# Kernel optimization log

Measured on AMD Instinct MI355X. Metric: run time of the kernel, lower is better.

## Reference

```python
import jax, jax.numpy as jnp
import numpy as np

BN_EPS = 1e-5


def conv1x1(x, w, b):
    # x: (B,C,H,W), w: (O,C), b: (O,)
    return jnp.einsum('bchw,oc->bohw', x, w) + b[None, :, None, None]


def maxpool2(x):
    # 2x2 max pool, stride 2; H,W assumed even
    B, C, H, W = x.shape
    return x.reshape(B, C, H // 2, 2, W // 2, 2).max(axis=(3, 5))


def setup_inputs() -> dict:
    key = jax.random.key(0)
    ks = jax.random.split(key, 8)
    B, C, Ci, H, W = 8, 256, 128, 64, 64
    s_in = 1.0 / np.sqrt(C)   # kaiming-uniform-ish scale for 1x1 convs
    s_ci = 1.0 / np.sqrt(Ci)
    return {
        'x': jax.random.normal(ks[0], (B, C, H, W), jnp.float32),
        'theta_w': jax.random.normal(ks[1], (Ci, C), jnp.float32) * s_in,
        'theta_b': jnp.zeros((Ci,), jnp.float32),
        'phi_w': jax.random.normal(ks[2], (Ci, C), jnp.float32) * s_in,
        'phi_b': jnp.zeros((Ci,), jnp.float32),
        'g_w': jax.random.normal(ks[3], (Ci, C), jnp.float32) * s_in,
        'g_b': jnp.zeros((Ci,), jnp.float32),
        'W_w': jax.random.normal(ks[4], (C, Ci), jnp.float32) * s_ci,
        'W_b': jnp.zeros((C,), jnp.float32),
        'bn_gamma': jnp.ones((C,), jnp.float32),
        'bn_beta': jnp.zeros((C,), jnp.float32),
    }


def reference(x, theta_w, theta_b, phi_w, phi_b, g_w, g_b, W_w, W_b, bn_gamma, bn_beta):
    B, C, H, W = x.shape
    Ci = theta_w.shape[0]
    # 1x1 conv projections
    theta = conv1x1(x, theta_w, theta_b).reshape(B, Ci, H * W)           # (B,Ci,N)
    phi = maxpool2(conv1x1(x, phi_w, phi_b)).reshape(B, Ci, -1)          # (B,Ci,M)
    g = maxpool2(conv1x1(x, g_w, g_b)).reshape(B, Ci, -1)                # (B,Ci,M)
    # attention: softmax(theta^T phi) g^T
    attn = jax.nn.softmax(jnp.einsum('bcn,bcm->bnm', theta, phi), axis=-1)  # (B,N,M)
    y = jnp.einsum('bnm,bcm->bcn', attn, g).reshape(B, Ci, H, W)
    # output projection + BatchNorm2d (training-mode batch stats) + residual
    y = conv1x1(y, W_w, W_b)
    mean = y.mean(axis=(0, 2, 3))
    var = y.var(axis=(0, 2, 3))
    y = (y - mean[None, :, None, None]) * jax.lax.rsqrt(var + BN_EPS)[None, :, None, None]
    y = y * bn_gamma[None, :, None, None] + bn_beta[None, :, None, None]
    return x + y
```

## Files before the change

### kernel.cpp

```cpp
#include <hip/hip_runtime.h>

#define B_ 8
#define C_ 256
#define CI_ 128
#define N_ 4096
#define M_ 1024

typedef unsigned short u16;
typedef unsigned int u32;
typedef _Float16 f16x8 __attribute__((ext_vector_type(8)));
typedef _Float16 f16x4 __attribute__((ext_vector_type(4)));
typedef float f32x4 __attribute__((ext_vector_type(4)));
typedef u16 u16x4 __attribute__((ext_vector_type(4)));
typedef u16 u16x8 __attribute__((ext_vector_type(8)));

__device__ __forceinline__ u16 f2h(float f) {
    _Float16 h = (_Float16)f;
    u16 u;
    __builtin_memcpy(&u, &h, 2);
    return u;
}
__device__ __forceinline__ float h2f(u16 u) {
    _Float16 h;
    __builtin_memcpy(&h, &u, 2);
    return (float)h;
}
__device__ __forceinline__ f16x8 ldh8(const u16* p) {
    return *reinterpret_cast<const f16x8*>(p);
}
__device__ __forceinline__ f32x4 MFMAH(f16x8 a, f16x8 b, f32x4 c) {
    return __builtin_amdgcn_mfma_f32_16x16x32_f16(a, b, c, 0, 0, 0);
}
__device__ __forceinline__ f32x4 MFMA16(f16x4 a, f16x4 b, f32x4 c) {
    return __builtin_amdgcn_mfma_f32_16x16x16f16(a, b, c, 0, 0, 0);
}
__device__ __forceinline__ void gld16(const u16* g, u16* l) {
    __builtin_amdgcn_global_load_lds(
        (const __attribute__((address_space(1))) void*)g,
        (__attribute__((address_space(3))) void*)l, 16, 0, 0);
}


__global__ __launch_bounds__(256) void k_prep(
    const float* __restrict__ tw, const float* __restrict__ tb,
    const float* __restrict__ pw, const float* __restrict__ pb,
    const float* __restrict__ gw, const float* __restrict__ gb,
    const float* __restrict__ Ww,
    u16* __restrict__ wcf, float* __restrict__ bcat, u16* __restrict__ wwf) {
    int idx = blockIdx.x * 256 + threadIdx.x;
    if (idx < 384 * 256) {
        int r = idx >> 8, c = idx & 255;
        float v = (r < 128) ? tw[r * 256 + c]
                : (r < 256) ? pw[(r - 128) * 256 + c]
                            : gw[(r - 256) * 256 + c];
        size_t off = (size_t)((r >> 4) * 8 + (c >> 5)) * 512 +
                     (((c >> 3) & 3) * 16 + (r & 15)) * 8 + (c & 7);
        wcf[off] = f2h(v);
    } else if (idx < 384 * 256 + 256 * 128) {
        int k2 = idx - 384 * 256;
        int c = k2 >> 7, k = k2 & 127;
        size_t off = (size_t)((c >> 4) * 4 + (k >> 5)) * 512 +
                     (((k >> 3) & 3) * 16 + (c & 15)) * 8 + (k & 7);
        wwf[off] = f2h(Ww[k2]);
    } else if (idx < 384 * 256 + 256 * 128 + 384) {
        int r = idx - (384 * 256 + 256 * 128);
        bcat[r] = (r < 128) ? tb[r] : (r < 256) ? pb[r - 128] : gb[r - 256];
    }
}

__global__ __launch_bounds__(256) void k_tx(const float* __restrict__ x,
                                            u16* __restrict__ xbf) {
    int bid = blockIdx.x;
    int b = bid >> 8, rem = bid & 255, nt = rem >> 2, ct = rem & 3;
    int n0 = nt * 64, c0 = ct * 64;
    __shared__ u16 th_[64][66];
    int j = threadIdx.x & 63, i0 = threadIdx.x >> 6;
    for (int i = i0; i < 64; i += 4)
        th_[i][j] = f2h(x[((size_t)b * C_ + c0 + i) * N_ + n0 + j]);
    __syncthreads();
    int w = threadIdx.x >> 6, lane = threadIdx.x & 63;
    int l15 = lane & 15, g16 = lane >> 4;
    int s = w;
#pragma unroll
    for (int kk = 0; kk < 2; ++kk) {
        u16x8 hv;
#pragma unroll
        for (int e = 0; e < 8; ++e)
            hv[e] = th_[kk * 32 + g16 * 8 + e][s * 16 + l15];
        size_t off = ((size_t)(b * 256 + (n0 >> 4) + s) * 8 + (c0 >> 5) + kk) * 512 +
                     (size_t)lane * 8;
        *(u16x8*)&xbf[off] = hv;
    }
}

__global__ __launch_bounds__(256) void k_proj(
    const u16* __restrict__ wcf, const float* __restrict__ bcat,
    const u16* __restrict__ xbf,
    u16* __restrict__ thf, u16* __restrict__ ppf, u16* __restrict__ gpf) {
    int bid = blockIdx.x;
    int b = bid / 96, rem = bid % 96, rt = rem >> 5, nt = rem & 31;
    int tid = threadIdx.x;
    int w = tid >> 6, lane = tid & 63;
    int l15 = lane & 15, g16 = lane >> 4;
    int wr = (w >> 1) * 64, wc = (w & 1) * 64;
    int rbase = rt * 128 + wr, nbase = nt * 128 + wc;
    __shared__ u16 tl[128][132];
    f32x4 acc[4][4];
#pragma unroll
    for (int i = 0; i < 4; ++i)
#pragma unroll
        for (int j = 0; j < 4; ++j)
#pragma unroll
            for (int r = 0; r < 4; ++r) acc[i][j][r] = 0.f;
#pragma unroll
    for (int ks = 0; ks < 8; ++ks) {
        f16x8 a[4], bb[4];
#pragma unroll
        for (int i = 0; i < 4; ++i)
            a[i] = ldh8(&wcf[((size_t)((rbase >> 4) + i) * 8 + ks) * 512 + (size_t)lane * 8]);
#pragma unroll
        for (int j = 0; j < 4; ++j)
            bb[j] = ldh8(&xbf[((size_t)(b * 256 + (nbase >> 4) + j) * 8 + ks) * 512 +
                              (size_t)lane * 8]);
#pragma unroll
        for (int i = 0; i < 4; ++i)
#pragma unroll
            for (int j = 0; j < 4; ++j) acc[i][j] = MFMAH(a[i], bb[j], acc[i][j]);
    }
    if (rt == 0) {
#pragma unroll
        for (int i = 0; i < 4; ++i) {
            int lrow = wr + i * 16 + g16 * 4;
#pragma unroll
            for (int j = 0; j < 4; ++j) {
                u16x4 pk;
#pragma unroll
                for (int r = 0; r < 4; ++r)
                    pk[r] = f2h(acc[i][j][r] + bcat[lrow + r]);
                size_t off = ((size_t)(b * 256 + (nbase >> 4) + j) * 4 + (lrow >> 5)) * 512 +
                             (((lrow >> 3) & 3) * 16 + l15) * 8 + (lrow & 7);
                *reinterpret_cast<u16x4*>(&thf[off]) = pk;
            }
        }
    } else {
#pragma unroll
        for (int i = 0; i < 4; ++i) {
            int lrow = wr + i * 16 + g16 * 4;
#pragma unroll
            for (int j = 0; j < 4; ++j) {
                int n_loc = wc + j * 16 + l15;
                u16x4 pk;
#pragma unroll
                for (int r = 0; r < 4; ++r)
                    pk[r] = f2h(acc[i][j][r] + bcat[rt * 128 + lrow + r]);
                *reinterpret_cast<u16x4*>(&tl[n_loc][lrow]) = pk;
            }
        }
        __syncthreads();
        if (rt == 1) {
#pragma unroll
            for (int half = 0; half < 2; ++half) {
                int w2 = (tid >> 4) + half * 16;
                int c8 = tid & 15;
                u16x8 v0 = *(const u16x8*)&tl[2 * w2][c8 * 8];
                u16x8 v1 = *(const u16x8*)&tl[2 * w2 + 1][c8 * 8];
                u16x8 v2 = *(const u16x8*)&tl[64 + 2 * w2][c8 * 8];
                u16x8 v3 = *(const u16x8*)&tl[65 + 2 * w2][c8 * 8];
                u16x8 o;
#pragma unroll
                for (int e = 0; e < 8; ++e) {
                    float mx = fmaxf(fmaxf(h2f(v0[e]), h2f(v1[e])),
                                     fmaxf(h2f(v2[e]), h2f(v3[e])));
                    o[e] = f2h(mx);
                }
                size_t off = ((size_t)(((b * 32 + nt) * 2 + (w2 >> 4)) * 4 + (c8 >> 2)) * 64 +
                              (c8 & 3) * 16 + (w2 & 15)) * 8;
                *(u16x8*)&ppf[off] = o;
            }
        } else {
#pragma unroll
            for (int s = 0; s < 2; ++s) {
                int wg = (tid >> 7) + s * 2;
                int ci = tid & 127;
                u16x4 o0, o1;
#pragma unroll
                for (int e = 0; e < 4; ++e) {
                    int w2a = wg * 8 + e;
                    int w2b = wg * 8 + 4 + e;
                    float va = fmaxf(fmaxf(h2f(tl[2 * w2a][ci]), h2f(tl[2 * w2a + 1][ci])),
                                     fmaxf(h2f(tl[64 + 2 * w2a][ci]), h2f(tl[65 + 2 * w2a][ci])));
                    float vb = fmaxf(fmaxf(h2f(tl[2 * w2b][ci]), h2f(tl[2 * w2b + 1][ci])),
                                     fmaxf(h2f(tl[64 + 2 * w2b][ci]), h2f(tl[65 + 2 * w2b][ci])));
                    o0[e] = f2h(va);
                    o1[e] = f2h(vb);
                }
                size_t base = (size_t)(b * 32 + nt) * 4096 +
                              (size_t)(((wg >> 1) * 8) + (ci >> 4)) * 256 + (ci & 15) * 4;
                *(u16x4*)&gpf[base + (((wg * 2) & 3) * 64)] = o0;
                *(u16x4*)&gpf[base + (((wg * 2 + 1) & 3) * 64)] = o1;
            }
        }
    }
}

__global__ __launch_bounds__(256) void k_attn(
    const u16* __restrict__ thf, const u16* __restrict__ ppf,
    const u16* __restrict__ gpf,
    u16* __restrict__ of, float2* __restrict__ ml) {
    int bid = blockIdx.x;
    int b = bid & 7, r = bid >> 3;
    int sp = r >> 6, nt = r & 63;
    int tid = threadIdx.x;
    int w = tid >> 6, lane = tid & 63;
    int l15 = lane & 15, g16 = lane >> 4;
    int n = nt * 64 + w * 16 + l15;
    int t16 = nt * 4 + w;
    __shared__ u16 kv[2][8192];

    f16x8 qf[4];
#pragma unroll
    for (int ks = 0; ks < 4; ++ks)
        qf[ks] = ldh8(&thf[((size_t)(b * 256 + t16) * 4 + ks) * 512 + (size_t)lane * 8]);

    f32x4 o[8];
#pragma unroll
    for (int ct = 0; ct < 8; ++ct)
#pragma unroll
        for (int rr = 0; rr < 4; ++rr) o[ct][rr] = 0.f;
    float mrun = -1e30f, lpart = 0.f;

    int itg0 = sp * 16;
    int soff = w * 512 + lane * 8;
    auto stage = [&](int bufidx, int itg) {
        const u16* ps = &ppf[(size_t)(b * 32 + itg) * 4096];
        const u16* gs = &gpf[(size_t)(b * 32 + itg) * 4096];
        u16* kb = &kv[bufidx][w * 512];
        gld16(ps + soff, kb);
        gld16(ps + 2048 + soff, kb + 2048);
        gld16(gs + soff, kb + 4096);
        gld16(gs + 2048 + soff, kb + 6144);
    };
    stage(0, itg0);
    __syncthreads();
    int cur = 0;

    for (int it = 0; it < 16; ++it) {
        if (it < 15) stage(cur ^ 1, itg0 + it + 1);
        f32x4 s0 = {0.f, 0.f, 0.f, 0.f}, s1 = {0.f, 0.f, 0.f, 0.f};
        __builtin_amdgcn_s_setprio(1);
#pragma unroll
        for (int ks = 0; ks < 4; ++ks) {
            f16x8 pa0 = ldh8(&kv[cur][ks * 512 + lane * 8]);
            f16x8 pa1 = ldh8(&kv[cur][(4 + ks) * 512 + lane * 8]);
            s0 = MFMAH(pa0, qf[ks], s0);
            s1 = MFMAH(pa1, qf[ks], s1);
        }
        __builtin_amdgcn_s_setprio(0);
        float pm8 = s0[0];
#pragma unroll
        for (int rr = 1; rr < 4; ++rr) pm8 = fmaxf(pm8, s0[rr]);
#pragma unroll
        for (int rr = 0; rr < 4; ++rr) pm8 = fmaxf(pm8, s1[rr]);
        if (__any(pm8 > mrun + 8.0f)) {
            float pm = fmaxf(pm8, __shfl_xor(pm8, 16));
            pm = fmaxf(pm, __shfl_xor(pm, 32));
            float mnew = fmaxf(mrun, pm);
            float sc = __expf(mrun - mnew);
#pragma unroll
            for (int ct = 0; ct < 8; ++ct)
#pragma unroll
                for (int rr = 0; rr < 4; ++rr) o[ct][rr] *= sc;
            lpart *= sc;
            mrun = mnew;
        }
        f16x4 pb0, pb1;
#pragma unroll
        for (int rr = 0; rr < 4; ++rr) {
            float p0 = __expf(s0[rr] - mrun);
            float p1 = __expf(s1[rr] - mrun);
            lpart += p0 + p1;
            pb0[rr] = (_Float16)p0;
            pb1[rr] = (_Float16)p1;
        }
        __builtin_amdgcn_s_setprio(1);
#pragma unroll
        for (int ct = 0; ct < 8; ++ct) {
            f16x4 g0 = *reinterpret_cast<const f16x4*>(&kv[cur][4096 + ct * 256 + lane * 4]);
            f16x4 g1 = *reinterpret_cast<const f16x4*>(&kv[cur][6144 + ct * 256 + lane * 4]);
            o[ct] = MFMA16(g0, pb0, o[ct]);
            o[ct] = MFMA16(g1, pb1, o[ct]);
        }
        __builtin_amdgcn_s_setprio(0);
        __syncthreads();
        cur ^= 1;
    }
    float lcol = lpart + __shfl_xor(lpart, 16);
    lcol += __shfl_xor(lcol, 32);
    float linv = 1.f / lcol;
    size_t obase = ((size_t)(b * 2 + sp) * N_ + n) * CI_;
#pragma unroll
    for (int ct = 0; ct < 8; ++ct) {
        u16x4 pk;
#pragma unroll
        for (int rr = 0; rr < 4; ++rr) pk[rr] = f2h(o[ct][rr] * linv);
        *reinterpret_cast<u16x4*>(&of[obase + ct * 16 + g16 * 4]) = pk;
    }
    if (g16 == 0) ml[(size_t)(b * 2 + sp) * N_ + n] = make_float2(mrun, lcol);
}

__global__ __launch_bounds__(256) void k_wconv(
    const u16* __restrict__ wwf, const float* __restrict__ Wb,
    const u16* __restrict__ of, const float2* __restrict__ ml,
    u16* __restrict__ z) {
    int bid = blockIdx.x;
    int b = bid >> 6, rem = bid & 63, ct2 = rem >> 5, nt = rem & 31;
    int w = threadIdx.x >> 6, lane = threadIdx.x & 63;
    int l15 = lane & 15, g16 = lane >> 4;
    int nbase = nt * 128 + (w >> 1) * 64;
    int cbase = ct2 * 128 + (w & 1) * 64;
    const size_t spstride = (size_t)N_ * CI_;
    float wsp[4][2];
#pragma unroll
    for (int i = 0; i < 4; ++i) {
        int n = nbase + i * 16 + l15;
        float2 m0 = ml[(size_t)(b * 2 + 0) * N_ + n];
        float2 m1 = ml[(size_t)(b * 2 + 1) * N_ + n];
        float M = fmaxf(m0.x, m1.x);
        float w0 = __expf(m0.x - M) * m0.y;
        float w1 = __expf(m1.x - M) * m1.y;
        float invL = 1.f / (w0 + w1);
        wsp[i][0] = w0 * invL;
        wsp[i][1] = w1 * invL;
    }
    f32x4 acc[4][4];
#pragma unroll
    for (int i = 0; i < 4; ++i)
#pragma unroll
        for (int j = 0; j < 4; ++j)
#pragma unroll
            for (int r = 0; r < 4; ++r) acc[i][j][r] = 0.f;
#pragma unroll
    for (int ks = 0; ks < 4; ++ks) {
        f16x8 a[4], bb[4];
#pragma unroll
        for (int i = 0; i < 4; ++i) {
            int n = nbase + i * 16 + l15;
            size_t base = ((size_t)(b * 2) * N_ + n) * CI_ + ks * 32 + g16 * 8;
            u16x8 v0 = *(const u16x8*)&of[base];
            u16x8 v1 = *(const u16x8*)&of[base + spstride];
            f16x8 av;
#pragma unroll
            for (int e = 0; e < 8; ++e) {
                float vv = h2f(v0[e]) * wsp[i][0] + h2f(v1[e]) * wsp[i][1];
                av[e] = (_Float16)vv;
            }
            a[i] = av;
        }
#pragma unroll
        for (int j = 0; j < 4; ++j)
            bb[j] = ldh8(&wwf[((size_t)((cbase >> 4) + j) * 4 + ks) * 512 + (size_t)lane * 8]);
#pragma unroll
        for (int i = 0; i < 4; ++i)
#pragma unroll
            for (int j = 0; j < 4; ++j) acc[i][j] = MFMAH(a[i], bb[j], acc[i][j]);
    }
#pragma unroll
    for (int j = 0; j < 4; ++j) {
        int ch = cbase + j * 16 + l15;
        float bias = Wb[ch];
        size_t rowbase = ((size_t)b * C_ + ch) * N_;
#pragma unroll
        for (int i = 0; i < 4; ++i) {
            u16x4 pk;
#pragma unroll
            for (int r = 0; r < 4; ++r) pk[r] = f2h(acc[i][j][r] + bias);
            *reinterpret_cast<u16x4*>(&z[rowbase + nbase + i * 16 + g16 * 4]) = pk;
        }
    }
}

__global__ __launch_bounds__(256) void k_stats(
    const u16* __restrict__ z, const float* __restrict__ gamma,
    const float* __restrict__ beta, float* __restrict__ bnp) {
    int c = blockIdx.x;
    int tid = threadIdx.x;
    float s = 0.f, q = 0.f;
#pragma unroll
    for (int b = 0; b < B_; ++b) {
        size_t base = ((size_t)b * C_ + c) * N_ + tid * 16;
        u16x8 v0 = *(const u16x8*)&z[base];
        u16x8 v1 = *(const u16x8*)&z[base + 8];
#pragma unroll
        for (int e = 0; e < 8; ++e) {
            float v = h2f(v0[e]);
            s += v;
            q += v * v;
            float u = h2f(v1[e]);
            s += u;
            q += u * u;
        }
    }
#pragma unroll
    for (int off = 1; off <= 32; off <<= 1) {
        s += __shfl_xor(s, off);
        q += __shfl_xor(q, off);
    }
    __shared__ float ss[4], qq[4];
    int w = tid >> 6;
    if ((tid & 63) == 0) {
        ss[w] = s;
        qq[w] = q;
    }
    __syncthreads();
    if (tid == 0) {
        s = ss[0] + ss[1] + ss[2] + ss[3];
        q = qq[0] + qq[1] + qq[2] + qq[3];
        const float inv_n = 1.f / 32768.f;
        float mean = s * inv_n;
        float var = q * inv_n - mean * mean;
        float sc = gamma[c] * rsqrtf(var + 1e-5f);
        bnp[c] = sc;
        bnp[256 + c] = beta[c] - mean * sc;
    }
}

__global__ __launch_bounds__(256) void k_final(
    const float* __restrict__ x, const u16* __restrict__ z,
    const float* __restrict__ bnp, float* __restrict__ out) {
    int i4 = blockIdx.x * 256 + threadIdx.x;
    size_t flat = (size_t)i4 * 4;
    int c = (int)((flat >> 12) & 255);
    float sc = bnp[c], sh = bnp[256 + c];
    float4 xx = *(const float4*)&x[flat];
    u16x4 zz = *(const u16x4*)&z[flat];
    float4 oo;
    oo.x = xx.x + h2f(zz[0]) * sc + sh;
    oo.y = xx.y + h2f(zz[1]) * sc + sh;
    oo.z = xx.z + h2f(zz[2]) * sc + sh;
    oo.w = xx.w + h2f(zz[3]) * sc + sh;
    *(float4*)&out[flat] = oo;
}

extern "C" void kernel_launch(void* const* d_in, const int* in_sizes, int n_in,
                              void* d_out, int out_size, void* d_ws, size_t ws_size,
                              hipStream_t stream) {
    const float* x     = (const float*)d_in[0];
    const float* tw    = (const float*)d_in[1];
    const float* tb    = (const float*)d_in[2];
    const float* pw    = (const float*)d_in[3];
    const float* pb    = (const float*)d_in[4];
    const float* gw    = (const float*)d_in[5];
    const float* gb    = (const float*)d_in[6];
    const float* Ww    = (const float*)d_in[7];
    const float* Wb    = (const float*)d_in[8];
    const float* gamma = (const float*)d_in[9];
    const float* beta  = (const float*)d_in[10];
    float* out = (float*)d_out;

    char* p = (char*)d_ws;
    auto alloc = [&](size_t bytes) {
        char* r = p;
        p += (bytes + 255) & ~(size_t)255;
        return r;
    };
    u16* xbf   = (u16*)alloc((size_t)B_ * N_ * C_ * 2);
    u16* thf   = (u16*)alloc((size_t)B_ * N_ * CI_ * 2);
    u16* ppf   = (u16*)alloc((size_t)B_ * M_ * CI_ * 2);
    u16* gpf   = (u16*)alloc((size_t)B_ * M_ * CI_ * 2);
    float2* ml = (float2*)alloc((size_t)2 * B_ * N_ * 8);
    u16* of    = (u16*)alloc((size_t)2 * B_ * N_ * CI_ * 2);
    u16* z     = (u16*)alloc((size_t)B_ * C_ * N_ * 2);
    u16* wcf   = (u16*)alloc(384 * 256 * 2);
    u16* wwf   = (u16*)alloc(256 * 128 * 2);
    float* bcat = (float*)alloc(384 * 4);
    float* bnp  = (float*)alloc(512 * 4);

    k_prep<<<514, 256, 0, stream>>>(tw, tb, pw, pb, gw, gb, Ww, wcf, bcat, wwf);
    k_tx<<<2048, 256, 0, stream>>>(x, xbf);
    k_proj<<<768, 256, 0, stream>>>(wcf, bcat, xbf, thf, ppf, gpf);
    k_attn<<<1024, 256, 0, stream>>>(thf, ppf, gpf, of, ml);
    k_wconv<<<512, 256, 0, stream>>>(wwf, Wb, of, ml, z);
    k_stats<<<256, 256, 0, stream>>>(z, gamma, beta, bnp);
    k_final<<<8192, 256, 0, stream>>>(x, z, bnp, out);
}
```

Before: 103.6 us.

## Load K/V tiles directly from global memory in attention kernel, dropping LDS staging

The attention kernel stops staging phi/g tiles through double-buffered LDS with async global-to-LDS loads and barriers. Each wave now reads its K and V fragments straight from global memory, relying on L2/L1 to serve the loads the four waves share. This removes the LDS allocation, the __syncthreads per iteration and the setprio hints, which should raise occupancy. In exchange it loses explicit prefetch overlap and adds redundant global traffic across waves, so load latency may be exposed.

```diff
diff --git a/kernel.cpp b/kernel.cpp
--- a/kernel.cpp
+++ b/kernel.cpp
@@ -28,16 +28,14 @@
 __device__ __forceinline__ f16x8 ldh8(const u16* p) {
     return *reinterpret_cast<const f16x8*>(p);
 }
+__device__ __forceinline__ f16x4 ldh4(const u16* p) {
+    return *reinterpret_cast<const f16x4*>(p);
+}
 __device__ __forceinline__ f32x4 MFMAH(f16x8 a, f16x8 b, f32x4 c) {
     return __builtin_amdgcn_mfma_f32_16x16x32_f16(a, b, c, 0, 0, 0);
 }
 __device__ __forceinline__ f32x4 MFMA16(f16x4 a, f16x4 b, f32x4 c) {
     return __builtin_amdgcn_mfma_f32_16x16x16f16(a, b, c, 0, 0, 0);
-}
-__device__ __forceinline__ void gld16(const u16* g, u16* l) {
-    __builtin_amdgcn_global_load_lds(
-        (const __attribute__((address_space(1))) void*)g,
-        (__attribute__((address_space(3))) void*)l, 16, 0, 0);
 }
 
 
@@ -215,7 +213,6 @@
     int l15 = lane & 15, g16 = lane >> 4;
     int n = nt * 64 + w * 16 + l15;
     int t16 = nt * 4 + w;
-    __shared__ u16 kv[2][8192];
 
     f16x8 qf[4];
 #pragma unroll
@@ -230,32 +227,17 @@
     float mrun = -1e30f, lpart = 0.f;
 
     int itg0 = sp * 16;
-    int soff = w * 512 + lane * 8;
-    auto stage = [&](int bufidx, int itg) {
-        const u16* ps = &ppf[(size_t)(b * 32 + itg) * 4096];
-        const u16* gs = &gpf[(size_t)(b * 32 + itg) * 4096];
-        u16* kb = &kv[bufidx][w * 512];
-        gld16(ps + soff, kb);
-        gld16(ps + 2048 + soff, kb + 2048);
-        gld16(gs + soff, kb + 4096);
-        gld16(gs + 2048 + soff, kb + 6144);
-    };
-    stage(0, itg0);
-    __syncthreads();
-    int cur = 0;
-
     for (int it = 0; it < 16; ++it) {
-        if (it < 15) stage(cur ^ 1, itg0 + it + 1);
+        const u16* pt = &ppf[(size_t)(b * 32 + itg0 + it) * 4096];
+        const u16* gt = &gpf[(size_t)(b * 32 + itg0 + it) * 4096];
         f32x4 s0 = {0.f, 0.f, 0.f, 0.f}, s1 = {0.f, 0.f, 0.f, 0.f};
-        __builtin_amdgcn_s_setprio(1);
 #pragma unroll
         for (int ks = 0; ks < 4; ++ks) {
-            f16x8 pa0 = ldh8(&kv[cur][ks * 512 + lane * 8]);
-            f16x8 pa1 = ldh8(&kv[cur][(4 + ks) * 512 + lane * 8]);
+            f16x8 pa0 = ldh8(&pt[ks * 512 + lane * 8]);
+            f16x8 pa1 = ldh8(&pt[(4 + ks) * 512 + lane * 8]);
             s0 = MFMAH(pa0, qf[ks], s0);
             s1 = MFMAH(pa1, qf[ks], s1);
         }
-        __builtin_amdgcn_s_setprio(0);
         float pm8 = s0[0];
 #pragma unroll
         for (int rr = 1; rr < 4; ++rr) pm8 = fmaxf(pm8, s0[rr]);
@@ -282,17 +264,13 @@
             pb0[rr] = (_Float16)p0;
             pb1[rr] = (_Float16)p1;
         }
-        __builtin_amdgcn_s_setprio(1);
 #pragma unroll
         for (int ct = 0; ct < 8; ++ct) {
-            f16x4 g0 = *reinterpret_cast<const f16x4*>(&kv[cur][4096 + ct * 256 + lane * 4]);
-            f16x4 g1 = *reinterpret_cast<const f16x4*>(&kv[cur][6144 + ct * 256 + lane * 4]);
+            f16x4 g0 = ldh4(&gt[ct * 256 + lane * 4]);
+            f16x4 g1 = ldh4(&gt[2048 + ct * 256 + lane * 4]);
             o[ct] = MFMA16(g0, pb0, o[ct]);
             o[ct] = MFMA16(g1, pb1, o[ct]);
         }
-        __builtin_amdgcn_s_setprio(0);
-        __syncthreads();
-        cur ^= 1;
     }
     float lcol = lpart + __shfl_xor(lpart, 16);
     lcol += __shfl_xor(lcol, 32);
```

New measurement: 121.5 us. 1.17x slower.

## Drop split-KV in attention; each block processes all keys, removing merge step

Applied to the files above, without the earlier changes.

The attention kernel no longer splits the 1024 keys into two halves across separate blocks. Each block now runs all 32 key tiles and writes the normalized output directly. This removes the partial-output and max/sum buffers and the softmax merge arithmetic in the W-conv kernel, cutting global traffic. The trade-off is half as many attention blocks (512 on a 256-CU device) with twice the serial loop length, which lowers parallelism and occupancy.

```diff
diff --git a/kernel.cpp b/kernel.cpp
--- a/kernel.cpp
+++ b/kernel.cpp
@@ -205,11 +205,9 @@
 
 __global__ __launch_bounds__(256) void k_attn(
     const u16* __restrict__ thf, const u16* __restrict__ ppf,
-    const u16* __restrict__ gpf,
-    u16* __restrict__ of, float2* __restrict__ ml) {
+    const u16* __restrict__ gpf, u16* __restrict__ ytf) {
     int bid = blockIdx.x;
-    int b = bid & 7, r = bid >> 3;
-    int sp = r >> 6, nt = r & 63;
+    int b = bid & 7, nt = bid >> 3;
     int tid = threadIdx.x;
     int w = tid >> 6, lane = tid & 63;
     int l15 = lane & 15, g16 = lane >> 4;
@@ -229,7 +227,6 @@
         for (int rr = 0; rr < 4; ++rr) o[ct][rr] = 0.f;
     float mrun = -1e30f, lpart = 0.f;
 
-    int itg0 = sp * 16;
     int soff = w * 512 + lane * 8;
     auto stage = [&](int bufidx, int itg) {
         const u16* ps = &ppf[(size_t)(b * 32 + itg) * 4096];
@@ -240,12 +237,12 @@
         gld16(gs + soff, kb + 4096);
         gld16(gs + 2048 + soff, kb + 6144);
     };
-    stage(0, itg0);
+    stage(0, 0);
     __syncthreads();
     int cur = 0;
 
-    for (int it = 0; it < 16; ++it) {
-        if (it < 15) stage(cur ^ 1, itg0 + it + 1);
+    for (int it = 0; it < 32; ++it) {
+        if (it < 31) stage(cur ^ 1, it + 1);
         f32x4 s0 = {0.f, 0.f, 0.f, 0.f}, s1 = {0.f, 0.f, 0.f, 0.f};
         __builtin_amdgcn_s_setprio(1);
 #pragma unroll
@@ -297,41 +294,25 @@
     float lcol = lpart + __shfl_xor(lpart, 16);
     lcol += __shfl_xor(lcol, 32);
     float linv = 1.f / lcol;
-    size_t obase = ((size_t)(b * 2 + sp) * N_ + n) * CI_;
+    size_t obase = ((size_t)b * N_ + n) * CI_;
 #pragma unroll
     for (int ct = 0; ct < 8; ++ct) {
         u16x4 pk;
 #pragma unroll
         for (int rr = 0; rr < 4; ++rr) pk[rr] = f2h(o[ct][rr] * linv);
-        *reinterpret_cast<u16x4*>(&of[obase + ct * 16 + g16 * 4]) = pk;
-    }
-    if (g16 == 0) ml[(size_t)(b * 2 + sp) * N_ + n] = make_float2(mrun, lcol);
+        *reinterpret_cast<u16x4*>(&ytf[obase + ct * 16 + g16 * 4]) = pk;
+    }
 }
 
 __global__ __launch_bounds__(256) void k_wconv(
     const u16* __restrict__ wwf, const float* __restrict__ Wb,
-    const u16* __restrict__ of, const float2* __restrict__ ml,
-    u16* __restrict__ z) {
+    const u16* __restrict__ ytf, u16* __restrict__ z) {
     int bid = blockIdx.x;
     int b = bid >> 6, rem = bid & 63, ct2 = rem >> 5, nt = rem & 31;
     int w = threadIdx.x >> 6, lane = threadIdx.x & 63;
     int l15 = lane & 15, g16 = lane >> 4;
     int nbase = nt * 128 + (w >> 1) * 64;
     int cbase = ct2 * 128 + (w & 1) * 64;
-    const size_t spstride = (size_t)N_ * CI_;
-    float wsp[4][2];
-#pragma unroll
-    for (int i = 0; i < 4; ++i) {
-        int n = nbase + i * 16 + l15;
-        float2 m0 = ml[(size_t)(b * 2 + 0) * N_ + n];
-        float2 m1 = ml[(size_t)(b * 2 + 1) * N_ + n];
-        float M = fmaxf(m0.x, m1.x);
-        float w0 = __expf(m0.x - M) * m0.y;
-        float w1 = __expf(m1.x - M) * m1.y;
-        float invL = 1.f / (w0 + w1);
-        wsp[i][0] = w0 * invL;
-        wsp[i][1] = w1 * invL;
-    }
     f32x4 acc[4][4];
 #pragma unroll
     for (int i = 0; i < 4; ++i)
@@ -345,16 +326,7 @@
 #pragma unroll
         for (int i = 0; i < 4; ++i) {
             int n = nbase + i * 16 + l15;
-            size_t base = ((size_t)(b * 2) * N_ + n) * CI_ + ks * 32 + g16 * 8;
-            u16x8 v0 = *(const u16x8*)&of[base];
-            u16x8 v1 = *(const u16x8*)&of[base + spstride];
-            f16x8 av;
-#pragma unroll
-            for (int e = 0; e < 8; ++e) {
-                float vv = h2f(v0[e]) * wsp[i][0] + h2f(v1[e]) * wsp[i][1];
-                av[e] = (_Float16)vv;
-            }
-            a[i] = av;
+            a[i] = ldh8(&ytf[((size_t)b * N_ + n) * CI_ + ks * 32 + g16 * 8]);
         }
 #pragma unroll
         for (int j = 0; j < 4; ++j)
@@ -467,8 +439,7 @@
     u16* thf   = (u16*)alloc((size_t)B_ * N_ * CI_ * 2);
     u16* ppf   = (u16*)alloc((size_t)B_ * M_ * CI_ * 2);
     u16* gpf   = (u16*)alloc((size_t)B_ * M_ * CI_ * 2);
-    float2* ml = (float2*)alloc((size_t)2 * B_ * N_ * 8);
-    u16* of    = (u16*)alloc((size_t)2 * B_ * N_ * CI_ * 2);
+    u16* ytf   = (u16*)alloc((size_t)B_ * N_ * CI_ * 2);
     u16* z     = (u16*)alloc((size_t)B_ * C_ * N_ * 2);
     u16* wcf   = (u16*)alloc(384 * 256 * 2);
     u16* wwf   = (u16*)alloc(256 * 128 * 2);
@@ -478,8 +449,8 @@
     k_prep<<<514, 256, 0, stream>>>(tw, tb, pw, pb, gw, gb, Ww, wcf, bcat, wwf);
     k_tx<<<2048, 256, 0, stream>>>(x, xbf);
     k_proj<<<768, 256, 0, stream>>>(wcf, bcat, xbf, thf, ppf, gpf);
-    k_attn<<<1024, 256, 0, stream>>>(thf, ppf, gpf, of, ml);
-    k_wconv<<<512, 256, 0, stream>>>(wwf, Wb, of, ml, z);
+    k_attn<<<512, 256, 0, stream>>>(thf, ppf, gpf, ytf);
+    k_wconv<<<512, 256, 0, stream>>>(wwf, Wb, ytf, z);
     k_stats<<<256, 256, 0, stream>>>(z, gamma, beta, bnp);
     k_final<<<8192, 256, 0, stream>>>(x, z, bnp, out);
 }
```

After: 97.86 us, median of 2. 5.5% less time.
